# Performance work log

Hardware: AMD Instinct MI355X
Metric: run time of the kernel (lower is better)

The kernel has to match this reference:

```python
import jax, jax.numpy as jnp
import numpy as np

DILATED_KS = (7, 7)   # dilated_kernel_size (Hk, Wk)
SCALING = 1.0
GROUPS = 1
STRIDE = (1, 1)
PADDING = (3, 3)


def construct_kernel(weight, P):
    """Bilinear scatter-add of kernel_count weighted points into a dense
    (out, in//g, Hk, Wk) kernel. weight: (O, Cg, K), P: (2, Cg, K)."""
    Hk, Wk = DILATED_KS
    lim_h, lim_w = Hk // 2, Wk // 2
    O, Cg, K = weight.shape
    ph = jnp.clip(P[0] * SCALING, -lim_h, lim_h) + lim_h    # (Cg, K) in [0, Hk-1]
    pw = jnp.clip(P[1] * SCALING, -lim_w, lim_w) + lim_w    # (Cg, K) in [0, Wk-1]
    ih = jnp.floor(ph).astype(jnp.int32)
    iw = jnp.floor(pw).astype(jnp.int32)
    rh = ph - ih
    rw = pw - iw
    cidx = jnp.broadcast_to(jnp.arange(Cg)[:, None], (Cg, K))
    kern = jnp.zeros((O, Cg, Hk, Wk), dtype=weight.dtype)
    corners = [(0, 0, (1 - rh) * (1 - rw)),
               (0, 1, (1 - rh) * rw),
               (1, 0, rh * (1 - rw)),
               (1, 1, rh * rw)]
    for di, dj, frac in corners:
        # out-of-range corners (at the boundary) have zero frac; 'drop' discards them
        kern = kern.at[:, cidx, ih + di, iw + dj].add(weight * frac[None], mode='drop')
    return kern


def setup_inputs() -> dict:
    key = jax.random.key(0)
    k1, k2, k3, k4 = jax.random.split(key, 4)
    x = jax.random.normal(k1, (32, 128, 56, 56), dtype=jnp.float32)
    weight = jax.random.normal(k2, (128, 128, 9), dtype=jnp.float32) * 0.05
    P = jax.random.normal(k3, (2, 128, 9), dtype=jnp.float32)  # positions ~ N(0,1), clamped in fwd
    bias = jax.random.normal(k4, (128,), dtype=jnp.float32) * 0.05
    return {"x": x, "weight": weight, "P": P, "bias": bias}


def reference(x, weight, P, bias):
    kern = construct_kernel(weight, P)  # (O, Cg, 7, 7)
    out = jax.lax.conv_general_dilated(
        x, kern,
        window_strides=STRIDE,
        padding=[(PADDING[0], PADDING[0]), (PADDING[1], PADDING[1])],
        dimension_numbers=('NCHW', 'OIHW', 'NCHW'),
        feature_group_count=GROUPS)
    return out + bias[None, :, None, None]
```

## Files before the change

kernel.cpp:

```cpp
#include <hip/hip_runtime.h>
#include <stdint.h>

typedef short v8s  __attribute__((ext_vector_type(8)));
typedef float v16f __attribute__((ext_vector_type(16)));

#define KS    7
#define KPTS  9
#define OCH   128
#define CCH   128
#define NB    32
#define HW    56
#define PAD   3

#define HBLK  8
#define ROWS  14
#define WP    72
#define CCK   32
#define NCC   4
#define HP    62
#define ROWB  (WP*CCK*2)
#define XS_B  (ROWS*ROWB)
#define AB_B  (8*4096*2)
#define SMEM_B (XS_B + AB_B)

__device__ __forceinline__ unsigned short f2bf(float f) {
  unsigned int u = __builtin_bit_cast(unsigned int, f);
  u += 0x7fffu + ((u >> 16) & 1u);
  return (unsigned short)(u >> 16);
}

__device__ __forceinline__ void gl_lds16(const void* g, void* l) {
  __builtin_amdgcn_global_load_lds(
      (const __attribute__((address_space(1))) unsigned int*)g,
      (__attribute__((address_space(3))) unsigned int*)l, 16, 0, 0);
}

__global__ __launch_bounds__(128) void build_kern(
    const float* __restrict__ wgt, const float* __restrict__ P,
    unsigned short* __restrict__ kb) {
  __shared__ float sm[OCH*49];
  const int c = blockIdx.x, o = threadIdx.x;
  float* mine = &sm[o*49];
  #pragma unroll
  for (int j = 0; j < 49; ++j) mine[j] = 0.f;
  for (int k = 0; k < KPTS; ++k) {
    const float ph = fminf(fmaxf(P[c*KPTS + k], -3.f), 3.f) + 3.f;
    const float pw = fminf(fmaxf(P[CCH*KPTS + c*KPTS + k], -3.f), 3.f) + 3.f;
    const int ih = (int)floorf(ph), iw = (int)floorf(pw);
    const float rh = ph - (float)ih, rw = pw - (float)iw;
    const float wt = wgt[(o*CCH + c)*KPTS + k];
    mine[ih*KS + iw] += wt*(1.f-rh)*(1.f-rw);
    if (iw+1 < KS) mine[ih*KS + iw+1] += wt*(1.f-rh)*rw;
    if (ih+1 < KS) mine[(ih+1)*KS + iw] += wt*rh*(1.f-rw);
    if (ih+1 < KS && iw+1 < KS) mine[(ih+1)*KS + iw+1] += wt*rh*rw;
  }
  const int cc = c >> 5, c32 = c & 31;
  const int kk = c32 >> 4, g = (c32 >> 3) & 1, j = c & 7;
  const int mt = o >> 5, l5 = o & 31;
  const size_t base = ((size_t)cc*49*8 + kk*4 + mt)*512 + (g*32 + l5)*8 + j;
  for (int tap = 0; tap < 49; ++tap)
    kb[base + (size_t)tap*4096] = f2bf(mine[tap]);
}

__global__ __launch_bounds__(256) void xpose(const float* __restrict__ x,
                                             unsigned short* __restrict__ xt) {
  __shared__ unsigned short lb[CCK][HW + 2];
  const int hp = blockIdx.x;
  const int cc = blockIdx.y;
  const int n  = blockIdx.z;
  const int t  = threadIdx.x;
  const int h  = hp - PAD;
  const bool valid = (unsigned)h < (unsigned)HW;
  if (valid) {
    const float* xb = x + ((size_t)(n*CCH + cc*CCK)*HW + h)*HW;
    #pragma unroll
    for (int k = 0; k < 7; ++k) {
      const int j = k*256 + t;
      const int c = j / HW, w = j % HW;
      lb[c][w] = f2bf(xb[(size_t)c*HW*HW + w]);
    }
  }
  __syncthreads();
  unsigned short* orow = xt + (size_t)((n*NCC + cc)*HP + hp)*(WP*4*8);
  for (int q = t; q < WP*4; q += 256) {
    const int kkg = q / WP, wq = q % WP;
    v8s v = (v8s){0,0,0,0,0,0,0,0};
    const int w = wq - PAD;
    if (valid && (unsigned)w < (unsigned)HW) {
      #pragma unroll
      for (int jj = 0; jj < 8; ++jj) v[jj] = (short)lb[kkg*8 + jj][w];
    }
    *(v8s*)&orow[q*8] = v;
  }
}

#define TAP_COMPUTE(T)                                                        \
  {                                                                           \
    const int kh = (T)/7, kw = (T) - kh*7;                                    \
    const unsigned short* ap = ab + (size_t)((T) & 7)*4096;                   \
    v8s a[8], b[2][4];                                                        \
    _Pragma("unroll")                                                         \
    for (int f = 0; f < 8; ++f)                                               \
      a[f] = *(const v8s*)&ap[f*512 + lane*8];                                \
    _Pragma("unroll")                                                         \
    for (int d = 0; d < 2; ++d) {                                             \
      const int r = wv*2 + d + kh;                                            \
      _Pragma("unroll")                                                       \
      for (int kk = 0; kk < 2; ++kk)                                          \
        _Pragma("unroll")                                                     \
        for (int nt = 0; nt < 2; ++nt)                                        \
          b[d][kk*2 + nt] = *(const v8s*)&xs[((size_t)((r*2 + kk)*2 + g)*WP + \
                                             nt*32 + kw + l5)*8];             \
    }                                                                         \
    __builtin_amdgcn_s_setprio(1);                                            \
    _Pragma("unroll")                                                         \
    for (int d = 0; d < 2; ++d)                                               \
      _Pragma("unroll")                                                       \
      for (int kk = 0; kk < 2; ++kk)                                          \
        _Pragma("unroll")                                                     \
        for (int mt = 0; mt < 4; ++mt)                                        \
          _Pragma("unroll")                                                   \
          for (int nt = 0; nt < 2; ++nt)                                      \
            acc[d][mt][nt] = __builtin_amdgcn_mfma_f32_32x32x16_bf16(         \
                a[kk*4 + mt], b[d][kk*2 + nt], acc[d][mt][nt], 0, 0, 0);      \
    __builtin_amdgcn_s_setprio(0);                                            \
  }

__global__ __launch_bounds__(256, 1) void dcls_conv(
    const unsigned short* __restrict__ xt, const unsigned short* __restrict__ kb,
    const float* __restrict__ bias, float* __restrict__ out)
{
  extern __shared__ char smem[];
  unsigned short* xs = (unsigned short*)smem;
  unsigned short* ab = (unsigned short*)(smem + XS_B);

  const int n   = blockIdx.x;
  const int hb  = blockIdx.y;
  const int tid = threadIdx.x;
  const int lane = tid & 63;
  const int wv   = tid >> 6;
  const int l5   = lane & 31;
  const int g    = lane >> 5;

  v16f acc[2][4][2];
  {
    v16f z;
    #pragma unroll
    for (int i = 0; i < 16; ++i) z[i] = 0.f;
    #pragma unroll
    for (int d = 0; d < 2; ++d)
      #pragma unroll
      for (int m = 0; m < 4; ++m)
        #pragma unroll
        for (int t = 0; t < 2; ++t)
          acc[d][m][t] = z;
  }

  for (int cc = 0; cc < NCC; ++cc) {
    const char* src = (const char*)xt + (size_t)((n*NCC + cc)*HP + hb*HBLK)*ROWB;
    for (int i = wv; i < 63; i += 4)
      gl_lds16(src + i*1024 + lane*16, (char*)xs + i*1024);
    const char* ks = (const char*)kb + (size_t)cc*49*8192;
    #pragma unroll
    for (int u = 0; u < 4; ++u)
      #pragma unroll
      for (int j = 0; j < 2; ++j)
        gl_lds16(ks + (size_t)u*8192 + (wv*2 + j)*1024 + lane*16,
                 (char*)ab + (size_t)u*8192 + (wv*2 + j)*1024);
    asm volatile("s_waitcnt vmcnt(0)" ::: "memory");
    __builtin_amdgcn_s_barrier();

    #pragma unroll 1
    for (int p = 0; p < 12; ++p) {
      const int tb = 4*p;
      #pragma unroll
      for (int j = 0; j < 4; ++j) {
        const int T = tb + 4 + j;
        if (T < 49) {
          #pragma unroll
          for (int q = 0; q < 2; ++q)
            gl_lds16(ks + (size_t)T*8192 + (wv*2 + q)*1024 + lane*16,
                     (char*)ab + (size_t)(T & 7)*8192 + (wv*2 + q)*1024);
        }
      }
      TAP_COMPUTE(tb)
      TAP_COMPUTE(tb + 1)
      TAP_COMPUTE(tb + 2)
      TAP_COMPUTE(tb + 3)
      asm volatile("s_waitcnt vmcnt(0)" ::: "memory");
      __builtin_amdgcn_s_barrier();
    }
    TAP_COMPUTE(48)
    __syncthreads();
  }

  #pragma unroll
  for (int d = 0; d < 2; ++d) {
    const int h = hb*HBLK + wv*2 + d;
    #pragma unroll
    for (int mt = 0; mt < 4; ++mt) {
      #pragma unroll
      for (int rr = 0; rr < 16; ++rr) {
        const int o = mt*32 + (rr & 3) + 8*(rr >> 2) + 4*g;
        const float bs = bias[o];
        out[((size_t)(n*OCH + o)*HW + h)*HW + l5] = acc[d][mt][0][rr] + bs;
        if (l5 < 24)
          out[((size_t)(n*OCH + o)*HW + h)*HW + 32 + l5] = acc[d][mt][1][rr] + bs;
      }
    }
  }
}

extern "C" void kernel_launch(void* const* d_in, const int* in_sizes, int n_in,
                              void* d_out, int out_size, void* d_ws, size_t ws_size,
                              hipStream_t stream) {
  const float* x    = (const float*)d_in[0];
  const float* wgt  = (const float*)d_in[1];
  const float* P    = (const float*)d_in[2];
  const float* bias = (const float*)d_in[3];
  float* out = (float*)d_out;

  unsigned short* kb = (unsigned short*)d_ws;
  unsigned short* xt = (unsigned short*)((char*)d_ws + (2u<<20));

  hipFuncSetAttribute((const void*)dcls_conv,
                      hipFuncAttributeMaxDynamicSharedMemorySize, SMEM_B);

  build_kern<<<CCH, OCH, 0, stream>>>(wgt, P, kb);
  xpose<<<dim3(HP, NCC, NB), 256, 0, stream>>>(x, xt);
  dcls_conv<<<dim3(NB, KS), 256, SMEM_B, stream>>>(xt, kb, bias, out);
}
```

Before: 175.7 us.

## Split conv block across 8 waves with one output row each and per-tap barriers

Doubles the conv block from 256 to 512 threads, so each wave computes one output row instead of two. This halves the accumulator registers per wave and gives each CU twice as many waves to hide LDS and MFMA latency. The per-tap compute is restructured into phases fenced by s_barrier and sched_barrier, which keeps waves in lockstep around LDS fragment loads and the buffered weight prefetch. In exchange, every wave now reloads the full A fragment, doubling LDS reads for weights, and two barriers per tap add synchronisation overhead.

Measured after the change: 176.5 us. No clear change (+0.4%).

```diff
diff --git a/kernel.cpp b/kernel.cpp
--- a/kernel.cpp
+++ b/kernel.cpp
@@ -20,7 +20,7 @@
 #define HP    62
 #define ROWB  (WP*CCK*2)
 #define XS_B  (ROWS*ROWB)
-#define AB_B  (8*4096*2)
+#define AB_B  (8*8192)
 #define SMEM_B (XS_B + AB_B)
 
 __device__ __forceinline__ unsigned short f2bf(float f) {
@@ -94,39 +94,44 @@
   }
 }
 
-#define TAP_COMPUTE(T)                                                        \
+#define TAP_PHASE(T, EXTRA)                                                   \
   {                                                                           \
     const int kh = (T)/7, kw = (T) - kh*7;                                    \
+    const int r = wv + kh;                                                    \
     const unsigned short* ap = ab + (size_t)((T) & 7)*4096;                   \
-    v8s a[8], b[2][4];                                                        \
+    v8s a[8], b[4];                                                           \
     _Pragma("unroll")                                                         \
     for (int f = 0; f < 8; ++f)                                               \
       a[f] = *(const v8s*)&ap[f*512 + lane*8];                                \
     _Pragma("unroll")                                                         \
-    for (int d = 0; d < 2; ++d) {                                             \
-      const int r = wv*2 + d + kh;                                            \
+    for (int kk = 0; kk < 2; ++kk)                                            \
       _Pragma("unroll")                                                       \
-      for (int kk = 0; kk < 2; ++kk)                                          \
+      for (int nt = 0; nt < 2; ++nt)                                          \
+        b[kk*2 + nt] = *(const v8s*)&xs[((size_t)((r*2 + kk)*2 + g)*WP +      \
+                                         nt*32 + kw + l5)*8];                 \
+    __builtin_amdgcn_sched_barrier(0);                                        \
+    __builtin_amdgcn_s_barrier();          \
+    __builtin_amdgcn_sched_barrier(0);                                        \
+    __builtin_amdgcn_s_setprio(1);                                            \
+    _Pragma("unroll")                                                         \
+    for (int kk = 0; kk < 2; ++kk)                                            \
+      _Pragma("unroll")                                                       \
+      for (int mt = 0; mt < 4; ++mt)                                          \
         _Pragma("unroll")                                                     \
         for (int nt = 0; nt < 2; ++nt)                                        \
-          b[d][kk*2 + nt] = *(const v8s*)&xs[((size_t)((r*2 + kk)*2 + g)*WP + \
-                                             nt*32 + kw + l5)*8];             \
-    }                                                                         \
-    __builtin_amdgcn_s_setprio(1);                                            \
-    _Pragma("unroll")                                                         \
-    for (int d = 0; d < 2; ++d)                                               \
-      _Pragma("unroll")                                                       \
-      for (int kk = 0; kk < 2; ++kk)                                          \
-        _Pragma("unroll")                                                     \
-        for (int mt = 0; mt < 4; ++mt)                                        \
-          _Pragma("unroll")                                                   \
-          for (int nt = 0; nt < 2; ++nt)                                      \
-            acc[d][mt][nt] = __builtin_amdgcn_mfma_f32_32x32x16_bf16(         \
-                a[kk*4 + mt], b[d][kk*2 + nt], acc[d][mt][nt], 0, 0, 0);      \
+          acc[mt][nt] = __builtin_amdgcn_mfma_f32_32x32x16_bf16(              \
+              a[kk*4 + mt], b[kk*2 + nt], acc[mt][nt], 0, 0, 0);              \
     __builtin_amdgcn_s_setprio(0);                                            \
-  }
-
-__global__ __launch_bounds__(256, 1) void dcls_conv(
+    __builtin_amdgcn_sched_barrier(0);                                        \
+    EXTRA                                                                     \
+    __builtin_amdgcn_s_barrier();           \
+    __builtin_amdgcn_sched_barrier(0);                                        \
+  }
+
+#define NOP_EXTRA
+#define VM0_EXTRA asm volatile("s_waitcnt vmcnt(0)" ::: "memory");
+
+__global__ __launch_bounds__(512, 2) void dcls_conv(
     const unsigned short* __restrict__ xt, const unsigned short* __restrict__ kb,
     const float* __restrict__ bias, float* __restrict__ out)
 {
@@ -142,31 +147,27 @@
   const int l5   = lane & 31;
   const int g    = lane >> 5;
 
-  v16f acc[2][4][2];
+  v16f acc[4][2];
   {
     v16f z;
     #pragma unroll
     for (int i = 0; i < 16; ++i) z[i] = 0.f;
     #pragma unroll
-    for (int d = 0; d < 2; ++d)
+    for (int m = 0; m < 4; ++m)
       #pragma unroll
-      for (int m = 0; m < 4; ++m)
-        #pragma unroll
-        for (int t = 0; t < 2; ++t)
-          acc[d][m][t] = z;
+      for (int t = 0; t < 2; ++t)
+        acc[m][t] = z;
   }
 
   for (int cc = 0; cc < NCC; ++cc) {
     const char* src = (const char*)xt + (size_t)((n*NCC + cc)*HP + hb*HBLK)*ROWB;
-    for (int i = wv; i < 63; i += 4)
+    for (int i = wv; i < 63; i += 8)
       gl_lds16(src + i*1024 + lane*16, (char*)xs + i*1024);
     const char* ks = (const char*)kb + (size_t)cc*49*8192;
     #pragma unroll
     for (int u = 0; u < 4; ++u)
-      #pragma unroll
-      for (int j = 0; j < 2; ++j)
-        gl_lds16(ks + (size_t)u*8192 + (wv*2 + j)*1024 + lane*16,
-                 (char*)ab + (size_t)u*8192 + (wv*2 + j)*1024);
+      gl_lds16(ks + (size_t)u*8192 + wv*1024 + lane*16,
+               (char*)ab + (size_t)u*8192 + wv*1024 + lane*16);
     asm volatile("s_waitcnt vmcnt(0)" ::: "memory");
     __builtin_amdgcn_s_barrier();
 
@@ -176,37 +177,28 @@
       #pragma unroll
       for (int j = 0; j < 4; ++j) {
         const int T = tb + 4 + j;
-        if (T < 49) {
-          #pragma unroll
-          for (int q = 0; q < 2; ++q)
-            gl_lds16(ks + (size_t)T*8192 + (wv*2 + q)*1024 + lane*16,
-                     (char*)ab + (size_t)(T & 7)*8192 + (wv*2 + q)*1024);
-        }
+        if (T < 49)
+          gl_lds16(ks + (size_t)T*8192 + wv*1024 + lane*16,
+                   (char*)ab + (size_t)(T & 7)*8192 + wv*1024 + lane*16);
       }
-      TAP_COMPUTE(tb)
-      TAP_COMPUTE(tb + 1)
-      TAP_COMPUTE(tb + 2)
-      TAP_COMPUTE(tb + 3)
-      asm volatile("s_waitcnt vmcnt(0)" ::: "memory");
-      __builtin_amdgcn_s_barrier();
-    }
-    TAP_COMPUTE(48)
-    __syncthreads();
-  }
-
+      TAP_PHASE(tb,     NOP_EXTRA)
+      TAP_PHASE(tb + 1, NOP_EXTRA)
+      TAP_PHASE(tb + 2, NOP_EXTRA)
+      TAP_PHASE(tb + 3, VM0_EXTRA)
+    }
+    TAP_PHASE(48, NOP_EXTRA)
+  }
+
+  const int h = hb*HBLK + wv;
   #pragma unroll
-  for (int d = 0; d < 2; ++d) {
-    const int h = hb*HBLK + wv*2 + d;
-    #pragma unroll
-    for (int mt = 0; mt < 4; ++mt) {
-      #pragma unroll
-      for (int rr = 0; rr < 16; ++rr) {
-        const int o = mt*32 + (rr & 3) + 8*(rr >> 2) + 4*g;
-        const float bs = bias[o];
-        out[((size_t)(n*OCH + o)*HW + h)*HW + l5] = acc[d][mt][0][rr] + bs;
-        if (l5 < 24)
-          out[((size_t)(n*OCH + o)*HW + h)*HW + 32 + l5] = acc[d][mt][1][rr] + bs;
-      }
+  for (int mt = 0; mt < 4; ++mt) {
+    #pragma unroll
+    for (int rr = 0; rr < 16; ++rr) {
+      const int o = mt*32 + (rr & 3) + 8*(rr >> 2) + 4*g;
+      const float bs = bias[o];
+      out[((size_t)(n*OCH + o)*HW + h)*HW + l5] = acc[mt][0][rr] + bs;
+      if (l5 < 24)
+        out[((size_t)(n*OCH + o)*HW + h)*HW + 32 + l5] = acc[mt][1][rr] + bs;
     }
   }
 }
@@ -228,5 +220,5 @@
 
   build_kern<<<CCH, OCH, 0, stream>>>(wgt, P, kb);
   xpose<<<dim3(HP, NCC, NB), 256, 0, stream>>>(x, xt);
-  dcls_conv<<<dim3(NB, KS), 256, SMEM_B, stream>>>(xt, kb, bias, out);
-}
+  dcls_conv<<<dim3(NB, KS), 512, SMEM_B, stream>>>(xt, kb, bias, out);
+}
```
